# Performance work log

Measured on AMD Instinct MI355X. Metric: run time of the kernel, lower is better.

## Reference

```python
import jax, jax.numpy as jnp
import numpy as np

RATIO = 0.1  # ratio_test == 0.1 branch of Crop.crop
B, L = 128, 262144
CROP_NUM = int(L * RATIO)          # 26214 samples removed per row
OUT_LEN = L - CROP_NUM             # 235930


def setup_inputs() -> dict:
    key = jax.random.key(0)
    k_audio, k_start = jax.random.split(key)
    audio = jax.random.normal(k_audio, (B, L), dtype=jnp.float32)
    # per-row random crop start, mirrors np.random.choice(range(0, L - crop_num - 1))
    starts = jax.random.randint(k_start, (B,), 0, L - CROP_NUM - 1, dtype=jnp.int32)
    return {"audio": audio, "starts": starts}


def reference(audio, starts):
    # out[i, j] = audio[i, j]             for j <  starts[i]
    # out[i, j] = audio[i, j + CROP_NUM]  for j >= starts[i]
    # Single fused gather instead of the per-row python loop + torch.cat chain.
    pos = jnp.arange(OUT_LEN, dtype=jnp.int32)                     # [OUT_LEN]
    idx = pos[None, :] + jnp.where(pos[None, :] >= starts[:, None], CROP_NUM, 0)  # [B, OUT_LEN]
    return jnp.take_along_axis(audio, idx, axis=1)
```

## Files before the change

### kernel.cpp

```cpp
#include <hip/hip_runtime.h>
#include <hip/hip_bf16.h>


constexpr int B_ = 128;
constexpr int L_ = 262144;
constexpr int CROP_ = 26214;
constexpr int OUT_LEN_ = L_ - CROP_;
constexpr long long TOTAL_ = (long long)B_ * OUT_LEN_;

__global__ __launch_bounds__(256) void crop_kernel(const float* __restrict__ audio,
                                                   const int* __restrict__ starts,
                                                   float* __restrict__ out) {
    long long t = (long long)blockIdx.x * blockDim.x + threadIdx.x;
    long long base = t * 4;
    if (base >= TOTAL_) return;

    int row = (int)(base / OUT_LEN_);
    long long row_base = (long long)row * OUT_LEN_;
    long long row_end  = row_base + OUT_LEN_;

    float r[4];
    if (base + 4 <= row_end) {
        int col = (int)(base - row_base);
        int s = starts[row];
        const float* src = audio + (long long)row * L_;
#pragma unroll
        for (int k = 0; k < 4; ++k) {
            int c = col + k;
            r[k] = src[c + (c >= s ? CROP_ : 0)];
        }
    } else {
#pragma unroll
        for (int k = 0; k < 4; ++k) {
            long long f = base + k;
            int rw = (int)(f / OUT_LEN_);
            int c = (int)(f - (long long)rw * OUT_LEN_);
            int s = starts[rw];
            r[k] = audio[(long long)rw * L_ + c + (c >= s ? CROP_ : 0)];
        }
    }
    *reinterpret_cast<float4*>(out + base) = make_float4(r[0], r[1], r[2], r[3]);
}

extern "C" void kernel_launch(void* const* d_in, const int* in_sizes, int n_in,
                              void* d_out, int out_size, void* d_ws, size_t ws_size,
                              hipStream_t stream) {
    const float* audio = (const float*)d_in[0];
    const int* starts  = (const int*)d_in[1];
    float* out = (float*)d_out;

    long long n_groups = TOTAL_ / 4;
    int block = 256;
    int grid = (int)((n_groups + block - 1) / block);
    crop_kernel<<<grid, block, 0, stream>>>(audio, starts, out);
}
```

Baseline: 224.7 us.

## Batch four float4 groups per thread with float2 vector loads and shared starts

Each thread now processes four strided groups of four outputs, issuing all loads before the stores so more memory requests are in flight. Non-straddling groups load as two float2 reads, since the source offset after a crop shift is only 2-element aligned, replacing four scalar loads. The starts array is staged in shared memory and index math moves to 32-bit unsigned to cut integer division cost. It adds a block-wide sync and higher register use per thread.

```diff
diff --git a/kernel.cpp b/kernel.cpp
--- a/kernel.cpp
+++ b/kernel.cpp
@@ -6,40 +6,67 @@
 constexpr int L_ = 262144;
 constexpr int CROP_ = 26214;
 constexpr int OUT_LEN_ = L_ - CROP_;
-constexpr long long TOTAL_ = (long long)B_ * OUT_LEN_;
+constexpr unsigned TOTAL_ = (unsigned)B_ * OUT_LEN_;
+constexpr unsigned NGROUPS_ = TOTAL_ / 4u;
+constexpr int GPT_ = 4;
 
 __global__ __launch_bounds__(256) void crop_kernel(const float* __restrict__ audio,
                                                    const int* __restrict__ starts,
                                                    float* __restrict__ out) {
-    long long t = (long long)blockIdx.x * blockDim.x + threadIdx.x;
-    long long base = t * 4;
-    if (base >= TOTAL_) return;
+    __shared__ int s_starts[B_];
+    if (threadIdx.x < B_) s_starts[threadIdx.x] = starts[threadIdx.x];
+    __syncthreads();
 
-    int row = (int)(base / OUT_LEN_);
-    long long row_base = (long long)row * OUT_LEN_;
-    long long row_end  = row_base + OUT_LEN_;
+    unsigned t = blockIdx.x * 256u + threadIdx.x;
+    unsigned stride = gridDim.x * 256u;
 
-    float r[4];
-    if (base + 4 <= row_end) {
-        int col = (int)(base - row_base);
-        int s = starts[row];
-        const float* src = audio + (long long)row * L_;
+    unsigned g[GPT_], row[GPT_], col[GPT_];
+    int s[GPT_];
+    bool ok[GPT_];
+    float2 a[GPT_], b[GPT_];
+
 #pragma unroll
-        for (int k = 0; k < 4; ++k) {
-            int c = col + k;
-            r[k] = src[c + (c >= s ? CROP_ : 0)];
-        }
-    } else {
+    for (int k = 0; k < GPT_; ++k) {
+        g[k] = t + (unsigned)k * stride;
+        ok[k] = g[k] < NGROUPS_;
+        unsigned base = ok[k] ? g[k] * 4u : 0u;
+        row[k] = base / (unsigned)OUT_LEN_;
+        col[k] = base - row[k] * (unsigned)OUT_LEN_;
+        s[k] = s_starts[row[k]];
+    }
+
 #pragma unroll
-        for (int k = 0; k < 4; ++k) {
-            long long f = base + k;
-            int rw = (int)(f / OUT_LEN_);
-            int c = (int)(f - (long long)rw * OUT_LEN_);
-            int s = starts[rw];
-            r[k] = audio[(long long)rw * L_ + c + (c >= s ? CROP_ : 0)];
+    for (int k = 0; k < GPT_; ++k) {
+        if (!ok[k]) continue;
+        unsigned c = col[k];
+        bool in_row   = (c + 4u <= (unsigned)OUT_LEN_);
+        bool straddle = ((int)c < s[k]) & ((int)c + 4 > s[k]);
+        if (in_row & !straddle) {
+            const float2* p = reinterpret_cast<const float2*>(
+                audio + (size_t)row[k] * L_ + c + ((int)c >= s[k] ? CROP_ : 0));
+            a[k] = p[0];
+            b[k] = p[1];
+        } else {
+            float r[4];
+#pragma unroll
+            for (int e = 0; e < 4; ++e) {
+                unsigned f = g[k] * 4u + (unsigned)e;
+                unsigned rw = f / (unsigned)OUT_LEN_;
+                int cc = (int)(f - rw * (unsigned)OUT_LEN_);
+                int ss = s_starts[rw];
+                r[e] = audio[(size_t)rw * L_ + cc + (cc >= ss ? CROP_ : 0)];
+            }
+            a[k] = make_float2(r[0], r[1]);
+            b[k] = make_float2(r[2], r[3]);
         }
     }
-    *reinterpret_cast<float4*>(out + base) = make_float4(r[0], r[1], r[2], r[3]);
+
+#pragma unroll
+    for (int k = 0; k < GPT_; ++k) {
+        if (!ok[k]) continue;
+        *reinterpret_cast<float4*>(out + (size_t)g[k] * 4u) =
+            make_float4(a[k].x, a[k].y, b[k].x, b[k].y);
+    }
 }
 
 extern "C" void kernel_launch(void* const* d_in, const int* in_sizes, int n_in,
@@ -49,8 +76,8 @@
     const int* starts  = (const int*)d_in[1];
     float* out = (float*)d_out;
 
-    long long n_groups = TOTAL_ / 4;
     int block = 256;
-    int grid = (int)((n_groups + block - 1) / block);
+    unsigned threads_needed = (NGROUPS_ + GPT_ - 1) / GPT_;
+    int grid = (int)((threads_needed + block - 1) / block);
     crop_kernel<<<grid, block, 0, stream>>>(audio, starts, out);
 }
```

New measurement: 230.1 us. 2.4% more time.
